# Kernel optimization log

Hardware: AMD Instinct MI355X
Metric: run time of the kernel (lower is better)

## Reference

```python
import jax, jax.numpy as jnp
import numpy as np

B, T, C, H = 4, 8192, 1024, 8
D = C // H  # head dim = 128

def setup_inputs() -> dict:
    key = jax.random.key(0)
    ks = jax.random.split(key, 9)
    s = 1.0 / np.sqrt(C)
    return {
        "x":  jax.random.normal(ks[0], (B, T, C), dtype=jnp.float32),
        "Wq": jax.random.normal(ks[1], (C, C), dtype=jnp.float32) * s,
        "bq": jax.random.normal(ks[2], (C,), dtype=jnp.float32) * s,
        "Wk": jax.random.normal(ks[3], (C, C), dtype=jnp.float32) * s,
        "bk": jax.random.normal(ks[4], (C,), dtype=jnp.float32) * s,
        "Wv": jax.random.normal(ks[5], (C, C), dtype=jnp.float32) * s,
        "bv": jax.random.normal(ks[6], (C,), dtype=jnp.float32) * s,
        "Wp": jax.random.normal(ks[7], (C, C), dtype=jnp.float32) * s,
        "bp": jax.random.normal(ks[8], (C,), dtype=jnp.float32) * s,
    }

def _heads(t):
    # [B, T, C] -> [B, H, T, D]
    return t.reshape(B, T, H, D).transpose(0, 2, 1, 3)

def reference(x, Wq, bq, Wk, bk, Wv, bv, Wp, bp):
    q = _heads(x @ Wq + bq)  # [B,H,T,D]
    k = _heads(x @ Wk + bk)
    v = _heads(x @ Wv + bv)
    # attn_type == 'l1': softmax over head/feature dim
    q = jax.nn.softmax(q, axis=-1)
    k = jax.nn.softmax(k, axis=-1)
    k_sum = k.sum(axis=-2, keepdims=True)                      # [B,H,1,D]
    D_inv = 1.0 / (q * k_sum).sum(axis=-1, keepdims=True)      # [B,H,T,1]
    context = jnp.einsum('bhtd,bhte->bhde', k, v)              # [B,H,D,D]
    y = jnp.einsum('bhtd,bhde->bhte', q, context) * D_inv + q  # [B,H,T,D]
    y = y.transpose(0, 2, 1, 3).reshape(B, T, C)               # merge heads
    return y @ Wp + bp
```

## Files before the change

kernel.cpp:

```cpp
#include <hip/hip_runtime.h>

#define B_ 4
#define T_ 8192
#define C_ 1024
#define H_ 8
#define D_ 128
#define M_ (B_*T_)
#define NKC_ 32

typedef __attribute__((ext_vector_type(8))) short bf16x8;
typedef __attribute__((ext_vector_type(4))) float f32x4;

__device__ __forceinline__ unsigned short f2b(float f) {
  union { float f; unsigned int u; } x; x.f = f;
  unsigned int r = x.u + 0x7fffu + ((x.u >> 16) & 1u);
  return (unsigned short)(r >> 16);
}
__device__ __forceinline__ float b2f(unsigned short u) {
  union { float f; unsigned int u; } x; x.u = ((unsigned int)u) << 16; return x.f;
}

__device__ __forceinline__ void gl2lds16(const void* g, void* l) {
  __builtin_amdgcn_global_load_lds((const __attribute__((address_space(1))) void*)g,
                                   (__attribute__((address_space(3))) void*)l, 16, 0, 0);
}

__device__ __forceinline__ int swz_id() {
  const int orig = blockIdx.y * 8 + blockIdx.x;
  return (orig & 7) * 256 + (orig >> 3);
}

template<typename OutT, bool VTRANS=false>
__global__ __launch_bounds__(256) void mfma_gemm_bias(
    const unsigned short* __restrict__ A,
    const unsigned short* __restrict__ Bt,
    const float* __restrict__ bias,
    OutT* __restrict__ out,
    int M, int N, int K)
{
  __shared__ __align__(16) char lds[65536];
  const int tid  = threadIdx.x;
  const int w    = tid >> 6, lane = tid & 63;
  const int id   = swz_id();
  const int bm   = (id >> 3) * 128, bn = (id & 7) * 128;
  const int wrow = (w >> 1) * 64, wcol = (w & 1) * 64;
  const int l15  = lane & 15, l4 = lane >> 4;
  const int srow = lane >> 3, sc = lane & 7;

  auto stage = [&](int buf, int k0) {
    char* As = lds + buf * 32768;
    char* Bs = As + 16384;
#pragma unroll
    for (int j = 0; j < 4; ++j) {
      const int ch  = w * 4 + j;
      const int row = ch * 8 + srow;
      const int kc  = sc ^ (row & 7);
      gl2lds16((const char*)(A  + (size_t)(bm + row) * K + k0) + kc * 16, As + ch * 1024 + lane * 16);
      gl2lds16((const char*)(Bt + (size_t)(bn + row) * K + k0) + kc * 16, Bs + ch * 1024 + lane * 16);
    }
  };

  f32x4 acc[4][4] = {};
  stage(0, 0);
  __syncthreads();
  int cur = 0;
  for (int k0 = 0; k0 < K; k0 += 64) {
    if (k0 + 64 < K) stage(cur ^ 1, k0 + 64);
    const char* As = lds + cur * 32768;
    const char* Bs = As + 16384;
#pragma unroll
    for (int ks = 0; ks < 2; ++ks) {
      bf16x8 af[4], bf[4];
#pragma unroll
      for (int i = 0; i < 4; ++i) {
        const int m  = wrow + i * 16 + l15;
        const int n  = wcol + i * 16 + l15;
        const int kc = ks * 4 + l4;
        af[i] = *(const bf16x8*)(As + m * 128 + ((kc ^ (m & 7)) * 16));
        bf[i] = *(const bf16x8*)(Bs + n * 128 + ((kc ^ (n & 7)) * 16));
      }
#pragma unroll
      for (int i = 0; i < 4; ++i)
#pragma unroll
        for (int j = 0; j < 4; ++j)
          acc[i][j] = __builtin_amdgcn_mfma_f32_16x16x32_bf16(af[i], bf[j], acc[i][j], 0, 0, 0);
    }
    __syncthreads();
    cur ^= 1;
  }

#pragma unroll
  for (int j = 0; j < 4; ++j) {
    const int col = bn + wcol + j * 16 + l15;
    const float bv = bias[col];
    if constexpr (VTRANS) {
      const int e = wcol + j * 16 + l15;
      const int h = bn >> 7;
#pragma unroll
      for (int i = 0; i < 4; ++i) {
        const int m = bm + wrow + i * 16 + l4 * 4;
        const int b = m >> 13, t = m & 8191;
        union { unsigned short u[4]; uint2 v; } pk;
#pragma unroll
        for (int r = 0; r < 4; ++r) pk.u[r] = f2b(acc[i][j][r] + bv);
        *(uint2*)((unsigned short*)out + ((size_t)(b * H_ + h) * D_ + e) * T_ + t) = pk.v;
      }
    } else {
#pragma unroll
      for (int i = 0; i < 4; ++i) {
        const int rbase = bm + wrow + i * 16 + l4 * 4;
#pragma unroll
        for (int r = 0; r < 4; ++r) {
          const float val = acc[i][j][r] + bv;
          if constexpr (sizeof(OutT) == 4)
            out[(size_t)(rbase + r) * N + col] = val;
          else
            ((unsigned short*)out)[(size_t)(rbase + r) * N + col] = f2b(val);
        }
      }
    }
  }
}

template<bool KMODE>
__global__ __launch_bounds__(256) void qk_gemm_softmax(
    const unsigned short* __restrict__ A,
    const unsigned short* __restrict__ Bt,
    const float* __restrict__ bias,
    unsigned short* __restrict__ kT,
    unsigned short* __restrict__ qb,
    float* __restrict__ ksum,
    const float* __restrict__ ksum_in,
    float* __restrict__ dinv)
{
  __shared__ __align__(16) char lds[65536];
  const int tid  = threadIdx.x;
  const int w    = tid >> 6, lane = tid & 63;
  const int id   = swz_id();
  const int bm   = (id >> 3) * 128, bn = (id & 7) * 128;
  const int wrow = w * 32;
  const int l15  = lane & 15, l4 = lane >> 4;
  const int srow = lane >> 3, sc = lane & 7;

  auto stage = [&](int buf, int k0) {
    char* As = lds + buf * 32768;
    char* Bs = As + 16384;
#pragma unroll
    for (int j = 0; j < 4; ++j) {
      const int ch  = w * 4 + j;
      const int row = ch * 8 + srow;
      const int kc  = sc ^ (row & 7);
      gl2lds16((const char*)(A  + (size_t)(bm + row) * 1024 + k0) + kc * 16, As + ch * 1024 + lane * 16);
      gl2lds16((const char*)(Bt + (size_t)(bn + row) * 1024 + k0) + kc * 16, Bs + ch * 1024 + lane * 16);
    }
  };

  f32x4 acc[2][8] = {};
  stage(0, 0);
  __syncthreads();
  int cur = 0;
  for (int k0 = 0; k0 < 1024; k0 += 64) {
    if (k0 + 64 < 1024) stage(cur ^ 1, k0 + 64);
    const char* As = lds + cur * 32768;
    const char* Bs = As + 16384;
#pragma unroll
    for (int ks = 0; ks < 2; ++ks) {
      bf16x8 af[2], bf[8];
      const int kc = ks * 4 + l4;
#pragma unroll
      for (int i = 0; i < 2; ++i) {
        const int m = wrow + i * 16 + l15;
        af[i] = *(const bf16x8*)(As + m * 128 + ((kc ^ (m & 7)) * 16));
      }
#pragma unroll
      for (int j = 0; j < 8; ++j) {
        const int n = j * 16 + l15;
        bf[j] = *(const bf16x8*)(Bs + n * 128 + ((kc ^ (n & 7)) * 16));
      }
#pragma unroll
      for (int i = 0; i < 2; ++i)
#pragma unroll
        for (int j = 0; j < 8; ++j)
          acc[i][j] = __builtin_amdgcn_mfma_f32_16x16x32_bf16(af[i], bf[j], acc[i][j], 0, 0, 0);
    }
    __syncthreads();
    cur ^= 1;
  }

  float bvj[8];
#pragma unroll
  for (int j = 0; j < 8; ++j) bvj[j] = bias[bn + j * 16 + l15];

#pragma unroll
  for (int i = 0; i < 2; ++i)
#pragma unroll
    for (int r = 0; r < 4; ++r) {
      float v[8];
      float mx = -1e30f;
#pragma unroll
      for (int j = 0; j < 8; ++j) { v[j] = acc[i][j][r] + bvj[j]; mx = fmaxf(mx, v[j]); }
#pragma unroll
      for (int off = 8; off > 0; off >>= 1) mx = fmaxf(mx, __shfl_xor(mx, off, 64));
      float s = 0.f;
#pragma unroll
      for (int j = 0; j < 8; ++j) { v[j] = expf(v[j] - mx); s += v[j]; }
#pragma unroll
      for (int off = 8; off > 0; off >>= 1) s += __shfl_xor(s, off, 64);
      const float inv = 1.0f / s;
#pragma unroll
      for (int j = 0; j < 8; ++j) acc[i][j][r] = v[j] * inv;
    }

  const int h  = bn >> 7;
  const int b  = bm >> 13;
  const int bh = b * 8 + h;

  if constexpr (KMODE) {
    float csum[8];
#pragma unroll
    for (int j = 0; j < 8; ++j) csum[j] = 0.f;
#pragma unroll
    for (int j = 0; j < 8; ++j) {
      const int d = j * 16 + l15;
#pragma unroll
      for (int i = 0; i < 2; ++i) {
        const int t = (bm + wrow + i * 16 + l4 * 4) & 8191;
        union { unsigned short u[4]; uint2 v2; } pk;
#pragma unroll
        for (int r = 0; r < 4; ++r) {
          const unsigned short us = f2b(acc[i][j][r]);
          pk.u[r] = us;
          csum[j] += b2f(us);
        }
        *(uint2*)(kT + ((size_t)bh * 128 + d) * 8192 + t) = pk.v2;
      }
    }
#pragma unroll
    for (int j = 0; j < 8; ++j) {
      csum[j] += __shfl_xor(csum[j], 16, 64);
      csum[j] += __shfl_xor(csum[j], 32, 64);
    }
    __syncthreads();
    float* red = (float*)lds;
    if (l4 == 0) {
#pragma unroll
      for (int j = 0; j < 8; ++j) red[w * 128 + j * 16 + l15] = csum[j];
    }
    __syncthreads();
    if (tid < 128) {
      const float s2 = red[tid] + red[128 + tid] + red[256 + tid] + red[384 + tid];
      atomicAdd(&ksum[(size_t)bh * 128 + tid], s2);
    }
  } else {
    float ks8[8];
#pragma unroll
    for (int j = 0; j < 8; ++j) ks8[j] = ksum_in[(size_t)bh * 128 + j * 16 + l15];
#pragma unroll
    for (int i = 0; i < 2; ++i)
#pragma unroll
      for (int r = 0; r < 4; ++r) {
        const int m = bm + wrow + i * 16 + l4 * 4 + r;
        float dot = 0.f;
#pragma unroll
        for (int j = 0; j < 8; ++j) {
          acc[i][j][r] = b2f(f2b(acc[i][j][r]));
          dot += acc[i][j][r] * ks8[j];
        }
#pragma unroll
        for (int off = 8; off > 0; off >>= 1) dot += __shfl_xor(dot, off, 64);
        if (l15 == 0) dinv[(size_t)bh * 8192 + (m & 8191)] = 1.0f / dot;
#pragma unroll
        for (int j = 0; j < 8; ++j)
          qb[(size_t)m * 1024 + bn + j * 16 + l15] = f2b(acc[i][j][r]);
      }
  }
}

__global__ __launch_bounds__(256) void ctx_part_mfma(
    const unsigned short* __restrict__ kT,
    const unsigned short* __restrict__ vT,
    float* __restrict__ part)
{
  __shared__ __align__(16) char lds[65536];
  const int tid  = threadIdx.x;
  const int w    = tid >> 6, lane = tid & 63;
  const int bh   = blockIdx.y;
  const int kbase = blockIdx.x * (T_ / NKC_);
  const int wrow = (w >> 1) * 64, wcol = (w & 1) * 64;
  const int l15  = lane & 15, l4 = lane >> 4;
  const int srow = lane >> 3, sc = lane & 7;
  const unsigned short* A  = kT + (size_t)bh * (D_ * T_);
  const unsigned short* Bt = vT + (size_t)bh * (D_ * T_);

  auto stage = [&](int buf, int k0) {
    char* As = lds + buf * 32768;
    char* Bs = As + 16384;
#pragma unroll
    for (int j = 0; j < 4; ++j) {
      const int ch  = w * 4 + j;
      const int row = ch * 8 + srow;
      const int kc  = sc ^ (row & 7);
      gl2lds16((const char*)(A  + (size_t)row * T_ + k0) + kc * 16, As + ch * 1024 + lane * 16);
      gl2lds16((const char*)(Bt + (size_t)row * T_ + k0) + kc * 16, Bs + ch * 1024 + lane * 16);
    }
  };

  f32x4 acc[4][4] = {};
  stage(0, kbase);
  __syncthreads();
  int cur = 0;
  for (int k0 = kbase; k0 < kbase + (T_ / NKC_); k0 += 64) {
    if (k0 + 64 < kbase + (T_ / NKC_)) stage(cur ^ 1, k0 + 64);
    const char* As = lds + cur * 32768;
    const char* Bs = As + 16384;
#pragma unroll
    for (int ks = 0; ks < 2; ++ks) {
      bf16x8 af[4], bf[4];
#pragma unroll
      for (int i = 0; i < 4; ++i) {
        const int m  = wrow + i * 16 + l15;
        const int n  = wcol + i * 16 + l15;
        const int kc = ks * 4 + l4;
        af[i] = *(const bf16x8*)(As + m * 128 + ((kc ^ (m & 7)) * 16));
        bf[i] = *(const bf16x8*)(Bs + n * 128 + ((kc ^ (n & 7)) * 16));
      }
#pragma unroll
      for (int i = 0; i < 4; ++i)
#pragma unroll
        for (int j = 0; j < 4; ++j)
          acc[i][j] = __builtin_amdgcn_mfma_f32_16x16x32_bf16(af[i], bf[j], acc[i][j], 0, 0, 0);
    }
    __syncthreads();
    cur ^= 1;
  }

  float* cb = part + ((size_t)blockIdx.x * 32 + bh) * (D_ * D_);
#pragma unroll
  for (int j = 0; j < 4; ++j) {
    const int e = wcol + j * 16 + l15;
#pragma unroll
    for (int i = 0; i < 4; ++i) {
      const int dbase = wrow + i * 16 + l4 * 4;
      *(f32x4*)&cb[(size_t)e * D_ + dbase] = acc[i][j];
    }
  }
}

__global__ __launch_bounds__(256) void ctx_reduce(
    const float* __restrict__ part, unsigned short* __restrict__ ctxTb)
{
  const size_t i = ((size_t)blockIdx.x * 256 + threadIdx.x) * 4;
  float4 a = {0.f, 0.f, 0.f, 0.f};
#pragma unroll 4
  for (int p = 0; p < NKC_; ++p) {
    float4 v = *(const float4*)(part + (size_t)p * (32 * D_ * D_) + i);
    a.x += v.x; a.y += v.y; a.z += v.z; a.w += v.w;
  }
  union { unsigned short u[4]; uint2 v2; } pk;
  pk.u[0] = f2b(a.x); pk.u[1] = f2b(a.y); pk.u[2] = f2b(a.z); pk.u[3] = f2b(a.w);
  *(uint2*)(ctxTb + i) = pk.v2;
}

__global__ __launch_bounds__(256) void y_mfma(
    const unsigned short* __restrict__ qb,
    const unsigned short* __restrict__ ctxTb,
    const float* __restrict__ dinv,
    unsigned short* __restrict__ yb)
{
  __shared__ __align__(16) char lds[65536];
  const int tid  = threadIdx.x;
  const int w    = tid >> 6, lane = tid & 63;
  const int id   = swz_id();
  const int bm   = (id >> 3) * 128, bn = (id & 7) * 128;
  const int wrow = (w >> 1) * 64, wcol = (w & 1) * 64;
  const int l15  = lane & 15, l4 = lane >> 4;
  const int srow = lane >> 3, sc = lane & 7;
  const int h = bn >> 7, b = bm >> 13, bh = b * 8 + h;
  const unsigned short* Bt = ctxTb + (size_t)bh * (D_ * D_);

  auto stage = [&](int buf, int k0) {
    char* As = lds + buf * 32768;
    char* Bs = As + 16384;
#pragma unroll
    for (int j = 0; j < 4; ++j) {
      const int ch  = w * 4 + j;
      const int row = ch * 8 + srow;
      const int kc  = sc ^ (row & 7);
      gl2lds16((const char*)(qb + (size_t)(bm + row) * 1024 + bn + k0) + kc * 16, As + ch * 1024 + lane * 16);
      gl2lds16((const char*)(Bt + (size_t)row * 128 + k0) + kc * 16, Bs + ch * 1024 + lane * 16);
    }
  };

  f32x4 acc[4][4] = {};
  stage(0, 0);
  __syncthreads();
  int cur = 0;
#pragma unroll
  for (int k0 = 0; k0 < 128; k0 += 64) {
    if (k0 + 64 < 128) stage(cur ^ 1, k0 + 64);
    const char* As = lds + cur * 32768;
    const char* Bs = As + 16384;
#pragma unroll
    for (int ks = 0; ks < 2; ++ks) {
      bf16x8 af[4], bf[4];
#pragma unroll
      for (int i = 0; i < 4; ++i) {
        const int m  = wrow + i * 16 + l15;
        const int n  = wcol + i * 16 + l15;
        const int kc = ks * 4 + l4;
        af[i] = *(const bf16x8*)(As + m * 128 + ((kc ^ (m & 7)) * 16));
        bf[i] = *(const bf16x8*)(Bs + n * 128 + ((kc ^ (n & 7)) * 16));
      }
#pragma unroll
      for (int i = 0; i < 4; ++i)
#pragma unroll
        for (int j = 0; j < 4; ++j)
          acc[i][j] = __builtin_amdgcn_mfma_f32_16x16x32_bf16(af[i], bf[j], acc[i][j], 0, 0, 0);
    }
    __syncthreads();
    cur ^= 1;
  }

  float di[4][4];
#pragma unroll
  for (int i = 0; i < 4; ++i)
#pragma unroll
    for (int r = 0; r < 4; ++r)
      di[i][r] = dinv[(size_t)bh * 8192 + ((bm + wrow + i * 16 + l4 * 4 + r) & 8191)];

#pragma unroll
  for (int j = 0; j < 4; ++j) {
    const int col = bn + wcol + j * 16 + l15;
#pragma unroll
    for (int i = 0; i < 4; ++i) {
      const int m = bm + wrow + i * 16 + l4 * 4;
#pragma unroll
      for (int r = 0; r < 4; ++r) {
        const float qv = b2f(qb[(size_t)(m + r) * 1024 + col]);
        yb[(size_t)(m + r) * 1024 + col] = f2b(fmaf(acc[i][j][r], di[i][r], qv));
      }
    }
  }
}

__global__ __launch_bounds__(256) void conv_bf16(
    const float* __restrict__ in, unsigned short* __restrict__ out)
{
  const size_t i = ((size_t)blockIdx.x * 256 + threadIdx.x) * 8;
  float4 a = *(const float4*)(in + i);
  float4 b = *(const float4*)(in + i + 4);
  union { unsigned short s[8]; uint4 v; } pk;
  pk.s[0] = f2b(a.x); pk.s[1] = f2b(a.y); pk.s[2] = f2b(a.z); pk.s[3] = f2b(a.w);
  pk.s[4] = f2b(b.x); pk.s[5] = f2b(b.y); pk.s[6] = f2b(b.z); pk.s[7] = f2b(b.w);
  *(uint4*)(out + i) = pk.v;
}

__global__ __launch_bounds__(256) void convT_w4(
    const float* __restrict__ W0, const float* __restrict__ W1,
    const float* __restrict__ W2, const float* __restrict__ W3,
    unsigned short* __restrict__ Wt0)
{
  const int z = blockIdx.z;
  const float* W = (z == 0) ? W0 : (z == 1) ? W1 : (z == 2) ? W2 : W3;
  unsigned short* Wt = Wt0 + (size_t)z * 1024 * 1024;
  __shared__ float s[32][33];
  const int k0 = blockIdx.x * 32, n0 = blockIdx.y * 32;
  const int tx = threadIdx.x & 31, ty = threadIdx.x >> 5;
#pragma unroll
  for (int r = ty; r < 32; r += 8) s[r][tx] = W[(size_t)(k0 + r) * 1024 + n0 + tx];
  __syncthreads();
#pragma unroll
  for (int r = ty; r < 32; r += 8) Wt[(size_t)(n0 + r) * 1024 + k0 + tx] = f2b(s[tx][r]);
}

extern "C" void kernel_launch(void* const* d_in, const int* in_sizes, int n_in,
                              void* d_out, int out_size, void* d_ws, size_t ws_size,
                              hipStream_t stream)
{
  const float* x  = (const float*)d_in[0];
  const float* Wq = (const float*)d_in[1];
  const float* bq = (const float*)d_in[2];
  const float* Wk = (const float*)d_in[3];
  const float* bk = (const float*)d_in[4];
  const float* Wv = (const float*)d_in[5];
  const float* bv = (const float*)d_in[6];
  const float* Wp = (const float*)d_in[7];
  const float* bp = (const float*)d_in[8];
  float* out = (float*)d_out;

  char* w = (char*)d_ws;
  unsigned short* xb  = (unsigned short*)w;
  unsigned short* qb  = (unsigned short*)(w + (64UL  << 20));
  unsigned short* kT  = (unsigned short*)(w + (128UL << 20));
  unsigned short* vT  = (unsigned short*)(w + (192UL << 20));
  unsigned short* Wtq = (unsigned short*)(w + (256UL << 20));
  unsigned short* Wtk = Wtq + 1024*1024;
  unsigned short* Wtv = Wtk + 1024*1024;
  unsigned short* Wtp = Wtv + 1024*1024;
  float* ksum  = (float*)(w + (264UL << 20));
  float* dinv  = (float*)(w + (265UL << 20));
  unsigned short* ctxTb = (unsigned short*)(w + (266UL << 20));
  float* part  = (float*)(w + (268UL << 20));
  unsigned short* yb = xb;

  hipMemsetAsync(ksum, 0, 16384, stream);

  dim3 blk(256);
  dim3 ggemm(C_/128, M_/128);

  conv_bf16<<<dim3(M_*C_/2048), blk, 0, stream>>>(x, xb);
  convT_w4<<<dim3(32, 32, 4), blk, 0, stream>>>(Wq, Wk, Wv, Wp, Wtq);

  qk_gemm_softmax<true><<<ggemm, blk, 0, stream>>>(xb, Wtk, bk, kT, nullptr, ksum, nullptr, nullptr);
  mfma_gemm_bias<unsigned short, true><<<ggemm, blk, 0, stream>>>(xb, Wtv, bv, vT, M_, C_, C_);
  qk_gemm_softmax<false><<<ggemm, blk, 0, stream>>>(xb, Wtq, bq, nullptr, qb, nullptr, ksum, dinv);

  ctx_part_mfma<<<dim3(NKC_, B_*H_), blk, 0, stream>>>(kT, vT, part);
  ctx_reduce   <<<dim3(32*D_*D_/1024), blk, 0, stream>>>(part, ctxTb);
  y_mfma<<<ggemm, blk, 0, stream>>>(qb, ctxTb, dinv, yb);

  mfma_gemm_bias<float><<<ggemm, blk, 0, stream>>>(yb, Wtp, bp, out, M_, C_, C_);
}
```

Before: 708.5 us.

## Deepen GEMM pipelines with two in-flight stages and partial vmcnt waits

Restructures the K-loop of all four MFMA GEMM kernels so two LDS tiles are prefetched up front. Each iteration waits only for the older tile's loads (vmcnt(8)) and then issues the next stage into the freed buffer after a release barrier, so the newer load stays in flight during compute. It also raises wave priority around the MFMA bursts with s_setprio. This relies on hand-placed waitcnt and sched_barrier and adds a second barrier per iteration.

```diff
diff --git a/kernel.cpp b/kernel.cpp
--- a/kernel.cpp
+++ b/kernel.cpp
@@ -23,6 +23,22 @@
 __device__ __forceinline__ void gl2lds16(const void* g, void* l) {
   __builtin_amdgcn_global_load_lds((const __attribute__((address_space(1))) void*)g,
                                    (__attribute__((address_space(3))) void*)l, 16, 0, 0);
+}
+
+__device__ __forceinline__ void pipe_wait8_barrier() {
+  asm volatile("s_waitcnt vmcnt(8)" ::: "memory");
+  __builtin_amdgcn_s_barrier();
+  __builtin_amdgcn_sched_barrier(0);
+}
+__device__ __forceinline__ void pipe_wait0_barrier() {
+  asm volatile("s_waitcnt vmcnt(0)" ::: "memory");
+  __builtin_amdgcn_s_barrier();
+  __builtin_amdgcn_sched_barrier(0);
+}
+__device__ __forceinline__ void pipe_release_barrier() {
+  __builtin_amdgcn_sched_barrier(0);
+  __builtin_amdgcn_s_barrier();
+  __builtin_amdgcn_sched_barrier(0);
 }
 
 __device__ __forceinline__ int swz_id() {
@@ -61,12 +77,8 @@
   };
 
   f32x4 acc[4][4] = {};
-  stage(0, 0);
-  __syncthreads();
-  int cur = 0;
-  for (int k0 = 0; k0 < K; k0 += 64) {
-    if (k0 + 64 < K) stage(cur ^ 1, k0 + 64);
-    const char* As = lds + cur * 32768;
+  auto compute = [&](int buf) {
+    const char* As = lds + buf * 32768;
     const char* Bs = As + 16384;
 #pragma unroll
     for (int ks = 0; ks < 2; ++ks) {
@@ -79,15 +91,29 @@
         af[i] = *(const bf16x8*)(As + m * 128 + ((kc ^ (m & 7)) * 16));
         bf[i] = *(const bf16x8*)(Bs + n * 128 + ((kc ^ (n & 7)) * 16));
       }
+      __builtin_amdgcn_s_setprio(1);
 #pragma unroll
       for (int i = 0; i < 4; ++i)
 #pragma unroll
         for (int j = 0; j < 4; ++j)
           acc[i][j] = __builtin_amdgcn_mfma_f32_16x16x32_bf16(af[i], bf[j], acc[i][j], 0, 0, 0);
-    }
-    __syncthreads();
+      __builtin_amdgcn_s_setprio(0);
+    }
+  };
+
+  const int nt = K >> 6;
+  stage(0, 0);
+  stage(1, 64);
+  int cur = 0;
+  for (int t = 0; t < nt - 1; ++t) {
+    pipe_wait8_barrier();
+    compute(cur);
+    pipe_release_barrier();
+    if (t + 2 < nt) stage(cur, (t + 2) << 6);
     cur ^= 1;
   }
+  pipe_wait0_barrier();
+  compute(cur);
 
 #pragma unroll
   for (int j = 0; j < 4; ++j) {
@@ -156,12 +182,8 @@
   };
 
   f32x4 acc[2][8] = {};
-  stage(0, 0);
-  __syncthreads();
-  int cur = 0;
-  for (int k0 = 0; k0 < 1024; k0 += 64) {
-    if (k0 + 64 < 1024) stage(cur ^ 1, k0 + 64);
-    const char* As = lds + cur * 32768;
+  auto compute = [&](int buf) {
+    const char* As = lds + buf * 32768;
     const char* Bs = As + 16384;
 #pragma unroll
     for (int ks = 0; ks < 2; ++ks) {
@@ -177,15 +199,28 @@
         const int n = j * 16 + l15;
         bf[j] = *(const bf16x8*)(Bs + n * 128 + ((kc ^ (n & 7)) * 16));
       }
+      __builtin_amdgcn_s_setprio(1);
 #pragma unroll
       for (int i = 0; i < 2; ++i)
 #pragma unroll
         for (int j = 0; j < 8; ++j)
           acc[i][j] = __builtin_amdgcn_mfma_f32_16x16x32_bf16(af[i], bf[j], acc[i][j], 0, 0, 0);
-    }
-    __syncthreads();
+      __builtin_amdgcn_s_setprio(0);
+    }
+  };
+
+  stage(0, 0);
+  stage(1, 64);
+  int cur = 0;
+  for (int t = 0; t < 15; ++t) {
+    pipe_wait8_barrier();
+    compute(cur);
+    pipe_release_barrier();
+    if (t + 2 < 16) stage(cur, (t + 2) << 6);
     cur ^= 1;
   }
+  pipe_wait0_barrier();
+  compute(cur);
 
   float bvj[8];
 #pragma unroll
@@ -306,12 +341,8 @@
   };
 
   f32x4 acc[4][4] = {};
-  stage(0, kbase);
-  __syncthreads();
-  int cur = 0;
-  for (int k0 = kbase; k0 < kbase + (T_ / NKC_); k0 += 64) {
-    if (k0 + 64 < kbase + (T_ / NKC_)) stage(cur ^ 1, k0 + 64);
-    const char* As = lds + cur * 32768;
+  auto compute = [&](int buf) {
+    const char* As = lds + buf * 32768;
     const char* Bs = As + 16384;
 #pragma unroll
     for (int ks = 0; ks < 2; ++ks) {
@@ -324,15 +355,28 @@
         af[i] = *(const bf16x8*)(As + m * 128 + ((kc ^ (m & 7)) * 16));
         bf[i] = *(const bf16x8*)(Bs + n * 128 + ((kc ^ (n & 7)) * 16));
       }
+      __builtin_amdgcn_s_setprio(1);
 #pragma unroll
       for (int i = 0; i < 4; ++i)
 #pragma unroll
         for (int j = 0; j < 4; ++j)
           acc[i][j] = __builtin_amdgcn_mfma_f32_16x16x32_bf16(af[i], bf[j], acc[i][j], 0, 0, 0);
-    }
-    __syncthreads();
+      __builtin_amdgcn_s_setprio(0);
+    }
+  };
+
+  stage(0, kbase);
+  stage(1, kbase + 64);
+  int cur = 0;
+  for (int t = 0; t < 3; ++t) {
+    pipe_wait8_barrier();
+    compute(cur);
+    pipe_release_barrier();
+    if (t + 2 < 4) stage(cur, kbase + ((t + 2) << 6));
     cur ^= 1;
   }
+  pipe_wait0_barrier();
+  compute(cur);
 
   float* cb = part + ((size_t)blockIdx.x * 32 + bh) * (D_ * D_);
 #pragma unroll
@@ -392,13 +436,8 @@
   };
 
   f32x4 acc[4][4] = {};
-  stage(0, 0);
-  __syncthreads();
-  int cur = 0;
-#pragma unroll
-  for (int k0 = 0; k0 < 128; k0 += 64) {
-    if (k0 + 64 < 128) stage(cur ^ 1, k0 + 64);
-    const char* As = lds + cur * 32768;
+  auto compute = [&](int buf) {
+    const char* As = lds + buf * 32768;
     const char* Bs = As + 16384;
 #pragma unroll
     for (int ks = 0; ks < 2; ++ks) {
@@ -411,15 +450,23 @@
         af[i] = *(const bf16x8*)(As + m * 128 + ((kc ^ (m & 7)) * 16));
         bf[i] = *(const bf16x8*)(Bs + n * 128 + ((kc ^ (n & 7)) * 16));
       }
+      __builtin_amdgcn_s_setprio(1);
 #pragma unroll
       for (int i = 0; i < 4; ++i)
 #pragma unroll
         for (int j = 0; j < 4; ++j)
           acc[i][j] = __builtin_amdgcn_mfma_f32_16x16x32_bf16(af[i], bf[j], acc[i][j], 0, 0, 0);
-    }
-    __syncthreads();
-    cur ^= 1;
-  }
+      __builtin_amdgcn_s_setprio(0);
+    }
+  };
+
+  stage(0, 0);
+  stage(1, 64);
+  pipe_wait8_barrier();
+  compute(0);
+  pipe_release_barrier();
+  pipe_wait0_barrier();
+  compute(1);
 
   float di[4][4];
 #pragma unroll
```

New measurement: 659.7 us. 1.07x faster.
